# Kernel tuning notes

Measured on AMD Instinct MI355X. Metric: run time of the kernel, lower is better.

Reference implementation:

```python
import jax, jax.numpy as jnp
import numpy as np
import math

HIDDEN = 4096
NUM_HEADS = 32
NUM_KV_HEADS = 8
HEAD_DIM = HIDDEN // NUM_HEADS          # 128
NUM_GROUPS = NUM_HEADS // NUM_KV_HEADS  # 4
BATCH, SEQ = 2, 2048


def setup_inputs() -> dict:
    key = jax.random.key(0)
    ks = jax.random.split(key, 5)
    s = 0.02
    return {
        "x":  jax.random.normal(ks[0], (BATCH, SEQ, HIDDEN), dtype=jnp.float32),
        "Wq": jax.random.normal(ks[1], (NUM_HEADS * HEAD_DIM, HIDDEN), dtype=jnp.float32) * s,
        "Wk": jax.random.normal(ks[2], (NUM_KV_HEADS * HEAD_DIM, HIDDEN), dtype=jnp.float32) * s,
        "Wv": jax.random.normal(ks[3], (NUM_KV_HEADS * HEAD_DIM, HIDDEN), dtype=jnp.float32) * s,
        "Wo": jax.random.normal(ks[4], (HIDDEN, HIDDEN), dtype=jnp.float32) * s,
    }


def reference(x, Wq, Wk, Wv, Wo):
    b, s, _ = x.shape
    # projections (nn.Linear: x @ W.T)
    q = (x @ Wq.T).reshape(b, s, NUM_KV_HEADS, NUM_GROUPS, HEAD_DIM)
    k = (x @ Wk.T).reshape(b, s, NUM_KV_HEADS, HEAD_DIM)
    v = (x @ Wv.T).reshape(b, s, NUM_KV_HEADS, HEAD_DIM)
    # q: [b, kv, g, q_len, d]; k/v: [b, kv, s, d]
    q = q.transpose(0, 2, 3, 1, 4)
    k = k.transpose(0, 2, 1, 3)
    v = v.transpose(0, 2, 1, 3)
    scale = 1.0 / math.sqrt(HEAD_DIM)
    # repeat_interleave(num_groups, dim=1) == grouped broadcast over g
    scores = jnp.einsum('bhgqd,bhkd->bhgqk', q, k) * scale
    causal = jnp.triu(jnp.ones((s, s), dtype=bool), k=1)  # full_len - seq_len + 1 = 1
    scores = jnp.where(causal, -jnp.inf, scores)
    attn = jax.nn.softmax(scores, axis=-1)
    out = jnp.einsum('bhgqk,bhkd->bhgqd', attn, v)
    # [b, kv, g, s, d] -> [b, s, kv*g*d] matching head order kv-major
    out = out.transpose(0, 3, 1, 2, 4).reshape(b, s, HIDDEN)
    return out @ Wo.T
```

## Files before the change

### kernel.cpp

```cpp
#include <hip/hip_runtime.h>
#include <hip/hip_bf16.h>

typedef __attribute__((ext_vector_type(8))) short bh8;
typedef __attribute__((ext_vector_type(4))) float fx4;
typedef __attribute__((ext_vector_type(4))) int ix4;
typedef __attribute__((ext_vector_type(2))) unsigned int ux2;

#define MFMA_BF16(a,b,c) __builtin_amdgcn_mfma_f32_16x16x32_bf16((a),(b),(c),0,0,0)

__device__ __forceinline__ unsigned short f2bf(float f){
  union { float f; unsigned u; } x; x.f = f;
  return (unsigned short)((x.u + 0x7fffu + ((x.u >> 16) & 1u)) >> 16);
}

__device__ __forceinline__ void gl_lds16(const void* g, void* l){
  typedef const void __attribute__((address_space(1)))* gp_t;
  typedef void __attribute__((address_space(3)))* lp_t;
  __builtin_amdgcn_global_load_lds((gp_t)g, (lp_t)l, 16, 0, 0);
}

__global__ __launch_bounds__(256) void cvt_kernel(const float* __restrict__ in,
                                                  unsigned short* __restrict__ out, int n){
  int i = (blockIdx.x * 256 + threadIdx.x) * 4;
  if (i >= n) return;
  float4 v = *reinterpret_cast<const float4*>(in + i);
  ushort4 o;
  o.x = f2bf(v.x); o.y = f2bf(v.y); o.z = f2bf(v.z); o.w = f2bf(v.w);
  *reinterpret_cast<ushort4*>(out + i) = o;
}

__global__ __launch_bounds__(256) void gemm_nt(const unsigned short* __restrict__ A,
                                               const unsigned short* __restrict__ B,
                                               void* __restrict__ Cout,
                                               int M, int N, int K, int out_f32){
  __shared__ __attribute__((aligned(16))) unsigned short As[128*32];
  __shared__ __attribute__((aligned(16))) unsigned short Bs[128*32];
  const int tid = threadIdx.x, lane = tid & 63, w = tid >> 6;
  const int row0 = blockIdx.x * 128, col0 = blockIdx.y * 128;
  const int wr = w >> 1, wc = w & 1;
  fx4 acc[4][4];
#pragma unroll
  for (int m=0;m<4;m++)
#pragma unroll
    for (int n=0;n<4;n++) acc[m][n] = (fx4){0.f,0.f,0.f,0.f};

  const int ldr = lane & 15;
  const int kb  = (lane >> 4) * 16;

  for (int k0 = 0; k0 < K; k0 += 32){
    __syncthreads();
#pragma unroll
    for (int i=0;i<2;i++){
      int chunk = w*2 + i;
      int r  = chunk*16 + (lane >> 2);
      int cb = (lane & 3) * 16;
      gl_lds16((const char*)A + ((size_t)(row0 + r)*K + k0)*2 + cb, (char*)As + chunk*1024);
      gl_lds16((const char*)B + ((size_t)(col0 + r)*K + k0)*2 + cb, (char*)Bs + chunk*1024);
    }
    __syncthreads();
    bh8 af[4], bf[4];
#pragma unroll
    for (int m=0;m<4;m++)
      af[m] = *reinterpret_cast<const bh8*>((const char*)As + (wr*64 + m*16 + ldr)*64 + kb);
#pragma unroll
    for (int n=0;n<4;n++)
      bf[n] = *reinterpret_cast<const bh8*>((const char*)Bs + (wc*64 + n*16 + ldr)*64 + kb);
#pragma unroll
    for (int m=0;m<4;m++)
#pragma unroll
      for (int n=0;n<4;n++)
        acc[m][n] = MFMA_BF16(af[m], bf[n], acc[m][n]);
  }
  const int er = (lane >> 4) * 4;
  const int ec = lane & 15;
  if (out_f32){
    float* C = (float*)Cout;
#pragma unroll
    for (int m=0;m<4;m++)
#pragma unroll
      for (int n=0;n<4;n++)
#pragma unroll
        for (int j=0;j<4;j++)
          C[(size_t)(row0 + wr*64 + m*16 + er + j)*N + (col0 + wc*64 + n*16 + ec)] = acc[m][n][j];
  } else {
    unsigned short* C = (unsigned short*)Cout;
#pragma unroll
    for (int m=0;m<4;m++)
#pragma unroll
      for (int n=0;n<4;n++)
#pragma unroll
        for (int j=0;j<4;j++)
          C[(size_t)(row0 + wr*64 + m*16 + er + j)*N + (col0 + wc*64 + n*16 + ec)] = f2bf(acc[m][n][j]);
  }
}

__global__ __launch_bounds__(256) void attn_kernel(const unsigned short* __restrict__ Q,
                                                   const unsigned short* __restrict__ Km,
                                                   const unsigned short* __restrict__ Vm,
                                                   unsigned short* __restrict__ O){
  __shared__ __attribute__((aligned(16))) unsigned short Ks[64*128];
  __shared__ __attribute__((aligned(16))) unsigned short Vt[128*64];
  __shared__ __attribute__((aligned(16))) unsigned short Ps[4][16*64];
  const int tid = threadIdx.x, lane = tid & 63, w = tid >> 6;
  const int g = lane >> 4, l15 = lane & 15;
  const int bq = (int)gridDim.x - 1 - (int)blockIdx.x;
  const int head = blockIdx.y;
  const int b = head >> 5, h = head & 31, kvh = h >> 2;
  const int q0 = bq*64 + w*16;
  const size_t tokbase = (size_t)b * 2048;
  const float C2 = 0.12751741104447086f;

  bh8 qf[4];
  {
    const char* qp = (const char*)Q + ((tokbase + q0 + l15)*4096 + h*128)*2;
#pragma unroll
    for (int kk=0;kk<4;kk++) qf[kk] = *reinterpret_cast<const bh8*>(qp + kk*64 + g*16);
  }
  float mrow = -1e38f, lrow = 0.f;
  fx4 acc[8];
#pragma unroll
  for (int f=0;f<8;f++) acc[f] = (fx4){0,0,0,0};

  const int ntile = bq + 1;
  for (int kt=0; kt<ntile; ++kt){
    const int kv0 = kt*64;
    __syncthreads();
#pragma unroll
    for (int i=0;i<4;i++){
      int r = i*16 + w*4 + (lane>>4);
      int c = (lane & 15) ^ (r & 7);
      gl_lds16((const char*)Km + ((tokbase + kv0 + r)*1024 + kvh*128)*2 + c*16,
               (char*)Ks + i*4096 + w*1024);
    }
    {
      int d = tid & 127, kh = tid >> 7;
      const unsigned short* vsrc = Vm + (tokbase + kv0 + kh*32)*1024 + kvh*128 + d;
#pragma unroll
      for (int half=0; half<2; ++half){
        unsigned int pk[8];
#pragma unroll
        for (int e=0;e<8;e++){
          unsigned int lo = vsrc[(size_t)(half*16 + 2*e)*1024];
          unsigned int hi = vsrc[(size_t)(half*16 + 2*e+1)*1024];
          pk[e] = lo | (hi << 16);
        }
#pragma unroll
        for (int c2=0;c2<2;c2++){
          ix4 vv; vv[0]=(int)pk[4*c2]; vv[1]=(int)pk[4*c2+1]; vv[2]=(int)pk[4*c2+2]; vv[3]=(int)pk[4*c2+3];
          *reinterpret_cast<ix4*>((char*)Vt + d*128 + ((kh*64 + half*32 + c2*16) ^ ((d&7)<<4))) = vv;
        }
      }
    }
    __syncthreads();
    fx4 s[4];
#pragma unroll
    for (int m=0;m<4;m++) s[m] = (fx4){0,0,0,0};
#pragma unroll
    for (int m=0;m<4;m++){
      const int kr = m*16 + l15;
#pragma unroll
      for (int kk=0;kk<4;kk++){
        bh8 kf = *reinterpret_cast<const bh8*>((const char*)Ks + kr*256 + ((kk*64 + g*16) ^ ((kr&7)<<4)));
        s[m] = MFMA_BF16(kf, qf[kk], s[m]);
      }
    }
    const int lim = q0 + l15 - kv0 - g*4;
#pragma unroll
    for (int m=0;m<4;m++)
#pragma unroll
      for (int j=0;j<4;j++)
        s[m][j] = (m*16 + j > lim) ? -1e30f : s[m][j]*C2;
    float mx = fmaxf(fmaxf(fmaxf(s[0][0],s[0][1]), fmaxf(s[0][2],s[0][3])),
                     fmaxf(fmaxf(s[1][0],s[1][1]), fmaxf(s[1][2],s[1][3])));
    mx = fmaxf(mx, fmaxf(fmaxf(fmaxf(s[2][0],s[2][1]), fmaxf(s[2][2],s[2][3])),
                         fmaxf(fmaxf(s[3][0],s[3][1]), fmaxf(s[3][2],s[3][3]))));
    mx = fmaxf(mx, __shfl_xor(mx, 16));
    mx = fmaxf(mx, __shfl_xor(mx, 32));
    if (__any(mx > mrow + 8.f)){
      float mnew = fmaxf(mrow, mx);
      float sc = exp2f(mrow - mnew);
      mrow = mnew;
      lrow *= sc;
      float sct[4];
#pragma unroll
      for (int j=0;j<4;j++) sct[j] = __shfl(sc, g*4 + j);
#pragma unroll
      for (int f=0;f<8;f++)
#pragma unroll
        for (int j=0;j<4;j++) acc[f][j] *= sct[j];
    }
    float rs = 0.f;
    ux2 pw[4];
#pragma unroll
    for (int m=0;m<4;m++){
      float p0 = exp2f(s[m][0]-mrow), p1 = exp2f(s[m][1]-mrow);
      float p2 = exp2f(s[m][2]-mrow), p3 = exp2f(s[m][3]-mrow);
      rs += (p0+p1)+(p2+p3);
      ux2 t; t[0] = (unsigned)f2bf(p0) | ((unsigned)f2bf(p1)<<16);
      t[1] = (unsigned)f2bf(p2) | ((unsigned)f2bf(p3)<<16);
      pw[m] = t;
    }
    rs += __shfl_xor(rs, 16);
    rs += __shfl_xor(rs, 32);
    lrow += rs;
#pragma unroll
    for (int m=0;m<4;m++)
      *reinterpret_cast<ux2*>((char*)&Ps[w][0] + l15*128 + ((m*32 + g*8) ^ ((l15&7)<<4))) = pw[m];
    asm volatile("s_waitcnt lgkmcnt(0)" ::: "memory");
#pragma unroll
    for (int t=0;t<2;t++){
      bh8 pa = *reinterpret_cast<const bh8*>((const char*)&Ps[w][0] + l15*128 + ((t*64 + g*16) ^ ((l15&7)<<4)));
#pragma unroll
      for (int f=0;f<8;f++){
        const int vr = f*16 + l15;
        bh8 vb = *reinterpret_cast<const bh8*>((const char*)Vt + vr*128 + ((t*64 + g*16) ^ ((vr&7)<<4)));
        acc[f] = MFMA_BF16(pa, vb, acc[f]);
      }
    }
  }
  {
    float inv[4];
#pragma unroll
    for (int j=0;j<4;j++) inv[j] = 1.f / __shfl(lrow, g*4 + j);
#pragma unroll
    for (int f=0;f<8;f++)
#pragma unroll
      for (int j=0;j<4;j++)
        O[(tokbase + q0 + g*4 + j)*4096 + h*128 + f*16 + l15] = f2bf(acc[f][j]*inv[j]);
  }
}

extern "C" void kernel_launch(void* const* d_in, const int* in_sizes, int n_in,
                              void* d_out, int out_size, void* d_ws, size_t ws_size,
                              hipStream_t stream){
  const float* x  = (const float*)d_in[0];
  const float* Wq = (const float*)d_in[1];
  const float* Wk = (const float*)d_in[2];
  const float* Wv = (const float*)d_in[3];
  const float* Wo = (const float*)d_in[4];
  char* ws = (char*)d_ws;
  const size_t MB = (size_t)1 << 20;
  unsigned short* xb  = (unsigned short*)(ws);
  unsigned short* Wqb = (unsigned short*)(ws + 32*MB);
  unsigned short* Wkb = (unsigned short*)(ws + 64*MB);
  unsigned short* Wvb = (unsigned short*)(ws + 72*MB);
  unsigned short* Qb  = (unsigned short*)(ws + 80*MB);
  unsigned short* Kb  = (unsigned short*)(ws + 112*MB);
  unsigned short* Vb  = (unsigned short*)(ws + 120*MB);

  const int NT = 2*2048;
  auto cvt = [&](const float* in, unsigned short* out, int n){
    cvt_kernel<<<dim3(n/1024), 256, 0, stream>>>(in, out, n);
  };
  cvt(x,  xb,  NT*4096);
  cvt(Wq, Wqb, 4096*4096);
  cvt(Wk, Wkb, 1024*4096);
  cvt(Wv, Wvb, 1024*4096);
  gemm_nt<<<dim3(32,32), 256, 0, stream>>>(xb, Wqb, Qb, NT, 4096, 4096, 0);
  gemm_nt<<<dim3(32, 8), 256, 0, stream>>>(xb, Wkb, Kb, NT, 1024, 4096, 0);
  gemm_nt<<<dim3(32, 8), 256, 0, stream>>>(xb, Wvb, Vb, NT, 1024, 4096, 0);
  cvt(Wo, Wqb, 4096*4096);
  attn_kernel<<<dim3(32,64), 256, 0, stream>>>(Qb, Kb, Vb, xb);
  gemm_nt<<<dim3(32,32), 256, 0, stream>>>(xb, Wqb, d_out, NT, 4096, 4096, 1);
}
```

Before: 1.090 ms.

## Fuse Q/K/V projections into one GEMM and add XCD-aware block swizzle

Concatenates the bf16 Wq, Wk and Wv weights so the three projections run as a single 4096x6144 GEMM writing an interleaved QKV buffer, which the attention kernel reads with a 6144 row stride. The GEMM grid becomes 1D with a block-index swizzle that spreads consecutive tile IDs across the chiplets. This removes two launches and the tail of the small K/V GEMMs and is meant to improve L2 reuse of A/B tiles. The strided QKV layout makes the attention loads of K and V less contiguous across rows.

Result: no change. 1.073 ms (-1.5%).

```diff
diff --git a/kernel.cpp b/kernel.cpp
--- a/kernel.cpp
+++ b/kernel.cpp
@@ -36,7 +36,12 @@
   __shared__ __attribute__((aligned(16))) unsigned short As[128*32];
   __shared__ __attribute__((aligned(16))) unsigned short Bs[128*32];
   const int tid = threadIdx.x, lane = tid & 63, w = tid >> 6;
-  const int row0 = blockIdx.x * 128, col0 = blockIdx.y * 128;
+  const int nby = N >> 7;
+  const int nwg = (int)gridDim.x;
+  const int id  = (int)blockIdx.x;
+  const int swz = (id & 7) * (nwg >> 3) + (id >> 3);
+  const int bx  = swz / nby, by = swz - bx*nby;
+  const int row0 = bx * 128, col0 = by * 128;
   const int wr = w >> 1, wc = w & 1;
   fx4 acc[4][4];
 #pragma unroll
@@ -98,6 +103,7 @@
                                                    const unsigned short* __restrict__ Km,
                                                    const unsigned short* __restrict__ Vm,
                                                    unsigned short* __restrict__ O){
+  const int QKS = 6144;
   __shared__ __attribute__((aligned(16))) unsigned short Ks[64*128];
   __shared__ __attribute__((aligned(16))) unsigned short Vt[128*64];
   __shared__ __attribute__((aligned(16))) unsigned short Ps[4][16*64];
@@ -112,7 +118,7 @@
 
   bh8 qf[4];
   {
-    const char* qp = (const char*)Q + ((tokbase + q0 + l15)*4096 + h*128)*2;
+    const char* qp = (const char*)Q + ((tokbase + q0 + l15)*QKS + h*128)*2;
 #pragma unroll
     for (int kk=0;kk<4;kk++) qf[kk] = *reinterpret_cast<const bh8*>(qp + kk*64 + g*16);
   }
@@ -129,19 +135,19 @@
     for (int i=0;i<4;i++){
       int r = i*16 + w*4 + (lane>>4);
       int c = (lane & 15) ^ (r & 7);
-      gl_lds16((const char*)Km + ((tokbase + kv0 + r)*1024 + kvh*128)*2 + c*16,
+      gl_lds16((const char*)Km + ((tokbase + kv0 + r)*QKS + kvh*128)*2 + c*16,
                (char*)Ks + i*4096 + w*1024);
     }
     {
       int d = tid & 127, kh = tid >> 7;
-      const unsigned short* vsrc = Vm + (tokbase + kv0 + kh*32)*1024 + kvh*128 + d;
+      const unsigned short* vsrc = Vm + (tokbase + kv0 + kh*32)*QKS + kvh*128 + d;
 #pragma unroll
       for (int half=0; half<2; ++half){
         unsigned int pk[8];
 #pragma unroll
         for (int e=0;e<8;e++){
-          unsigned int lo = vsrc[(size_t)(half*16 + 2*e)*1024];
-          unsigned int hi = vsrc[(size_t)(half*16 + 2*e+1)*1024];
+          unsigned int lo = vsrc[(size_t)(half*16 + 2*e)*QKS];
+          unsigned int hi = vsrc[(size_t)(half*16 + 2*e+1)*QKS];
           pk[e] = lo | (hi << 16);
         }
 #pragma unroll
@@ -240,26 +246,20 @@
   const float* Wo = (const float*)d_in[4];
   char* ws = (char*)d_ws;
   const size_t MB = (size_t)1 << 20;
-  unsigned short* xb  = (unsigned short*)(ws);
-  unsigned short* Wqb = (unsigned short*)(ws + 32*MB);
-  unsigned short* Wkb = (unsigned short*)(ws + 64*MB);
-  unsigned short* Wvb = (unsigned short*)(ws + 72*MB);
-  unsigned short* Qb  = (unsigned short*)(ws + 80*MB);
-  unsigned short* Kb  = (unsigned short*)(ws + 112*MB);
-  unsigned short* Vb  = (unsigned short*)(ws + 120*MB);
+  unsigned short* xb   = (unsigned short*)(ws);
+  unsigned short* Wb   = (unsigned short*)(ws + 32*MB);
+  unsigned short* QKVb = (unsigned short*)(ws + 80*MB);
 
   const int NT = 2*2048;
   auto cvt = [&](const float* in, unsigned short* out, int n){
     cvt_kernel<<<dim3(n/1024), 256, 0, stream>>>(in, out, n);
   };
-  cvt(x,  xb,  NT*4096);
-  cvt(Wq, Wqb, 4096*4096);
-  cvt(Wk, Wkb, 1024*4096);
-  cvt(Wv, Wvb, 1024*4096);
-  gemm_nt<<<dim3(32,32), 256, 0, stream>>>(xb, Wqb, Qb, NT, 4096, 4096, 0);
-  gemm_nt<<<dim3(32, 8), 256, 0, stream>>>(xb, Wkb, Kb, NT, 1024, 4096, 0);
-  gemm_nt<<<dim3(32, 8), 256, 0, stream>>>(xb, Wvb, Vb, NT, 1024, 4096, 0);
-  cvt(Wo, Wqb, 4096*4096);
-  attn_kernel<<<dim3(32,64), 256, 0, stream>>>(Qb, Kb, Vb, xb);
-  gemm_nt<<<dim3(32,32), 256, 0, stream>>>(xb, Wqb, d_out, NT, 4096, 4096, 1);
-}
+  cvt(x,  xb, NT*4096);
+  cvt(Wq, Wb,                     4096*4096);
+  cvt(Wk, Wb + (size_t)4096*4096, 1024*4096);
+  cvt(Wv, Wb + (size_t)5120*4096, 1024*4096);
+  gemm_nt<<<dim3(1536), 256, 0, stream>>>(xb, Wb, QKVb, NT, 6144, 4096, 0);
+  cvt(Wo, Wb, 4096*4096);
+  attn_kernel<<<dim3(32,64), 256, 0, stream>>>(QKVb, QKVb + 4096, QKVb + 5120, xb);
+  gemm_nt<<<dim3(1024), 256, 0, stream>>>(xb, Wb, d_out, NT, 4096, 4096, 1);
+}
```
